# Kernel optimization log

Measured on AMD Instinct MI355X. Metric: run time of the kernel, lower is better.

The kernel has to match this reference:

```python
import jax, jax.numpy as jnp
import numpy as np


def _per_sample_ce(logits, targets):
    # -log_softmax(logits)[i, targets[i]]  -> shape [N]
    logp = jax.nn.log_softmax(logits, axis=-1)
    return -jnp.take_along_axis(logp, targets[:, None], axis=-1)[:, 0]


def setup_inputs() -> dict:
    key = jax.random.key(0)
    k1, k2, k3 = jax.random.split(key, 3)
    N, C = 65536, 1000
    y_1 = jax.random.normal(k1, (N, C), dtype=jnp.float32)
    y_2 = jax.random.normal(k2, (N, C), dtype=jnp.float32)
    targets = jax.random.randint(k3, (N,), 0, C, dtype=jnp.int64)
    num_keep = 45875  # int(0.7 * N), static for jit
    return {"y_1": y_1, "y_2": y_2, "targets": targets, "num_keep": num_keep}


def reference(y_1, y_2, targets, num_keep):
    loss_1 = _per_sample_ce(y_1, targets)          # [N]
    loss_2 = _per_sample_ce(y_2, targets)          # [N]
    # small-loss selection: indices of the num_keep smallest per-sample losses
    ind_1_update = jnp.argsort(loss_1)[:num_keep]  # selected by net 1
    ind_2_update = jnp.argsort(loss_2)[:num_keep]  # selected by net 2
    # cross-update: each net trains on the peer's selected samples
    loss_1_update = _per_sample_ce(y_1[ind_2_update], targets[ind_2_update])
    loss_2_update = _per_sample_ce(y_2[ind_1_update], targets[ind_1_update])
    # size_average=True -> means
    return (loss_1_update.mean(), loss_2_update.mean(),
            loss_1.mean(), loss_2.mean())
```

## Files before the change

kernel.cpp:

```cpp
#include <hip/hip_runtime.h>
#include <math.h>

#define MAXT 2048

__device__ __forceinline__ unsigned keyOf(float f) {
  unsigned b = __float_as_uint(f);
  return b ^ ((b & 0x80000000u) ? 0xFFFFFFFFu : 0x80000000u);
}

__device__ __forceinline__ float waveMax(float v) {
#pragma unroll
  for (int o = 32; o >= 1; o >>= 1) v = fmaxf(v, __shfl_xor(v, o));
  return v;
}
__device__ __forceinline__ float waveSum(float v) {
#pragma unroll
  for (int o = 32; o >= 1; o >>= 1) v += __shfl_xor(v, o);
  return v;
}

__device__ __forceinline__ void selectStep(const unsigned* __restrict__ h,
                                           int per, unsigned rank,
                                           unsigned* sc, unsigned* res) {
  int t = threadIdx.x;
  unsigned local[8];
  unsigned s = 0;
  for (int j = 0; j < per; ++j) { local[j] = h[t * per + j]; s += local[j]; }
  sc[t] = s;
  __syncthreads();
  for (int off = 1; off < 256; off <<= 1) {
    unsigned v = (t >= off) ? sc[t - off] : 0u;
    __syncthreads();
    sc[t] += v;
    __syncthreads();
  }
  unsigned incl = sc[t], excl = incl - s;
  if (excl < rank && rank <= incl) {
    unsigned cum = excl;
    for (int j = 0; j < per; ++j) {
      if (cum + local[j] >= rank) {
        res[0] = (unsigned)(t * per + j);
        res[1] = rank - cum;
        break;
      }
      cum += local[j];
    }
  }
  __syncthreads();
}

__global__ __launch_bounds__(256) void init_kernel(unsigned* __restrict__ hbase,
                                                   unsigned* __restrict__ tc) {
  int t = threadIdx.x;
  for (int j = t; j < 2 * (2048 + 2048 + 1024); j += 256) hbase[j] = 0u;
  if (t < 2) tc[t] = 0u;
}

__global__ __launch_bounds__(256) void ce_kernel(
    const float* __restrict__ y1, const float* __restrict__ y2,
    const int* __restrict__ tgt,
    float* __restrict__ l1, float* __restrict__ l2, int N) {
  const float L2E = 1.4426950408889634f;
  const float LN2 = 0.6931471805599453f;
  int wid = threadIdx.x >> 6, lane = threadIdx.x & 63;
  int row = blockIdx.x * 4 + wid;
  if (row >= N) return;
  int t = tgt[row];
  int vecIdx = t >> 2;
  int grp = vecIdx >> 6;
  int srcLane = vecIdx & 63;
  int comp = t & 3;
#pragma unroll
  for (int which = 0; which < 2; ++which) {
    const float* y = which ? y2 : y1;
    const float4* rp = (const float4*)(y + (size_t)row * 1000);
    float4 a = rp[lane];
    float4 b = rp[lane + 64];
    float4 c = rp[lane + 128];
    float4 d = make_float4(-INFINITY, -INFINITY, -INFINITY, -INFINITY);
    if (lane + 192 < 250) d = rp[lane + 192];
    float4 sel = (grp == 0) ? a : (grp == 1) ? b : (grp == 2) ? c : d;
    float cand = (comp == 0) ? sel.x : (comp == 1) ? sel.y
               : (comp == 2) ? sel.z : sel.w;
    float xt = __shfl(cand, srcLane);
    float m = fmaxf(fmaxf(fmaxf(a.x, a.y), fmaxf(a.z, a.w)),
                    fmaxf(fmaxf(b.x, b.y), fmaxf(b.z, b.w)));
    m = fmaxf(m, fmaxf(fmaxf(c.x, c.y), fmaxf(c.z, c.w)));
    m = fmaxf(m, fmaxf(fmaxf(d.x, d.y), fmaxf(d.z, d.w)));
    m = waveMax(m);
    float s = exp2f((a.x - m) * L2E) + exp2f((a.y - m) * L2E) +
              exp2f((a.z - m) * L2E) + exp2f((a.w - m) * L2E) +
              exp2f((b.x - m) * L2E) + exp2f((b.y - m) * L2E) +
              exp2f((b.z - m) * L2E) + exp2f((b.w - m) * L2E) +
              exp2f((c.x - m) * L2E) + exp2f((c.y - m) * L2E) +
              exp2f((c.z - m) * L2E) + exp2f((c.w - m) * L2E) +
              exp2f((d.x - m) * L2E) + exp2f((d.y - m) * L2E) +
              exp2f((d.z - m) * L2E) + exp2f((d.w - m) * L2E);
    s = waveSum(s);
    if (lane == 0) {
      float loss = log2f(s) * LN2 + m - xt;
      (which ? l2 : l1)[row] = loss;
    }
  }
}

__global__ __launch_bounds__(256) void histA_kernel(
    const float* __restrict__ l1, const float* __restrict__ l2,
    unsigned* __restrict__ hA1, unsigned* __restrict__ hA2, int N) {
  __shared__ unsigned lh[2][2048];
  int t = threadIdx.x;
  for (int j = t; j < 2048; j += 256) { lh[0][j] = 0u; lh[1][j] = 0u; }
  __syncthreads();
  for (int i = blockIdx.x * blockDim.x + t; i < N;
       i += gridDim.x * blockDim.x) {
    atomicAdd(&lh[0][keyOf(l1[i]) >> 21], 1u);
    atomicAdd(&lh[1][keyOf(l2[i]) >> 21], 1u);
  }
  __syncthreads();
  for (int j = t; j < 2048; j += 256) {
    unsigned v0 = lh[0][j], v1 = lh[1][j];
    if (v0) atomicAdd(&hA1[j], v0);
    if (v1) atomicAdd(&hA2[j], v1);
  }
}

__global__ __launch_bounds__(256) void histB_kernel(
    const float* __restrict__ l1, const float* __restrict__ l2,
    const unsigned* __restrict__ hA1, const unsigned* __restrict__ hA2,
    unsigned* __restrict__ hB1, unsigned* __restrict__ hB2,
    const int* __restrict__ numKeep, int N) {
  __shared__ unsigned sc[256];
  __shared__ unsigned resA1[2], resA2[2];
  unsigned k0 = (unsigned)(*numKeep);
  selectStep(hA1, 8, k0, sc, resA1);
  selectStep(hA2, 8, k0, sc, resA2);
  unsigned a1 = resA1[0], a2 = resA2[0];
  for (int i = blockIdx.x * blockDim.x + threadIdx.x; i < N;
       i += gridDim.x * blockDim.x) {
    unsigned k1 = keyOf(l1[i]);
    if ((k1 >> 21) == a1) atomicAdd(&hB1[(k1 >> 10) & 2047u], 1u);
    unsigned k2 = keyOf(l2[i]);
    if ((k2 >> 21) == a2) atomicAdd(&hB2[(k2 >> 10) & 2047u], 1u);
  }
}

__global__ __launch_bounds__(256) void histC_kernel(
    const float* __restrict__ l1, const float* __restrict__ l2,
    const unsigned* __restrict__ hA1, const unsigned* __restrict__ hA2,
    const unsigned* __restrict__ hB1, const unsigned* __restrict__ hB2,
    unsigned* __restrict__ hC1, unsigned* __restrict__ hC2,
    const int* __restrict__ numKeep, int N) {
  __shared__ unsigned sc[256];
  __shared__ unsigned rA1[2], rA2[2], rB1[2], rB2[2];
  unsigned k0 = (unsigned)(*numKeep);
  selectStep(hA1, 8, k0, sc, rA1);
  selectStep(hA2, 8, k0, sc, rA2);
  selectStep(hB1, 8, rA1[1], sc, rB1);
  selectStep(hB2, 8, rA2[1], sc, rB2);
  unsigned p1 = (rA1[0] << 21) | (rB1[0] << 10);
  unsigned p2 = (rA2[0] << 21) | (rB2[0] << 10);
  for (int i = blockIdx.x * blockDim.x + threadIdx.x; i < N;
       i += gridDim.x * blockDim.x) {
    unsigned k1 = keyOf(l1[i]);
    if ((k1 & 0xFFFFFC00u) == p1) atomicAdd(&hC1[k1 & 1023u], 1u);
    unsigned k2 = keyOf(l2[i]);
    if ((k2 & 0xFFFFFC00u) == p2) atomicAdd(&hC2[k2 & 1023u], 1u);
  }
}

__global__ __launch_bounds__(256) void partial_kernel(
    const float* __restrict__ l1, const float* __restrict__ l2,
    const unsigned* __restrict__ hA1, const unsigned* __restrict__ hA2,
    const unsigned* __restrict__ hB1, const unsigned* __restrict__ hB2,
    const unsigned* __restrict__ hC1, const unsigned* __restrict__ hC2,
    const int* __restrict__ numKeep, unsigned* __restrict__ needs,
    unsigned* __restrict__ tc, int* __restrict__ tIdx1, float* __restrict__ tVal1,
    int* __restrict__ tIdx2, float* __restrict__ tVal2,
    float* __restrict__ partials, int N) {
  __shared__ unsigned sc[256];
  __shared__ unsigned rA1[2], rA2[2], rB1[2], rB2[2], rC1[2], rC2[2];
  unsigned k0 = (unsigned)(*numKeep);
  selectStep(hA1, 8, k0, sc, rA1);
  selectStep(hA2, 8, k0, sc, rA2);
  selectStep(hB1, 8, rA1[1], sc, rB1);
  selectStep(hB2, 8, rA2[1], sc, rB2);
  selectStep(hC1, 4, rB1[1], sc, rC1);
  selectStep(hC2, 4, rB2[1], sc, rC2);
  unsigned K1 = (rA1[0] << 21) | (rB1[0] << 10) | rC1[0];
  unsigned K2 = (rA2[0] << 21) | (rB2[0] << 10) | rC2[0];
  if (threadIdx.x == 0) { needs[0] = rC1[1]; needs[1] = rC2[1]; }
  float s0 = 0.f, s1 = 0.f, s2 = 0.f, s3 = 0.f;
  for (int i = blockIdx.x * blockDim.x + threadIdx.x; i < N;
       i += gridDim.x * blockDim.x) {
    float f1 = l1[i], f2 = l2[i];
    unsigned k1 = keyOf(f1), k2 = keyOf(f2);
    if (k2 < K2) {
      s0 += f1;
    } else if (k2 == K2) {
      unsigned p = atomicAdd(&tc[1], 1u);
      if (p < MAXT) { tIdx2[p] = i; tVal2[p] = f1; }
    }
    if (k1 < K1) {
      s1 += f2;
    } else if (k1 == K1) {
      unsigned p = atomicAdd(&tc[0], 1u);
      if (p < MAXT) { tIdx1[p] = i; tVal1[p] = f2; }
    }
    s2 += f1;
    s3 += f2;
  }
  s0 = waveSum(s0); s1 = waveSum(s1); s2 = waveSum(s2); s3 = waveSum(s3);
  __shared__ float red[4][4];
  int wid = threadIdx.x >> 6, lane = threadIdx.x & 63;
  if (lane == 0) {
    red[wid][0] = s0; red[wid][1] = s1; red[wid][2] = s2; red[wid][3] = s3;
  }
  __syncthreads();
  if (threadIdx.x == 0) {
    for (int q = 0; q < 4; ++q)
      partials[blockIdx.x * 4 + q] =
          red[0][q] + red[1][q] + red[2][q] + red[3][q];
  }
}

__global__ __launch_bounds__(256) void final_kernel(
    const float* __restrict__ partials, const int* __restrict__ numKeep,
    const unsigned* __restrict__ needs, const unsigned* __restrict__ tc,
    const int* __restrict__ tIdx1, const float* __restrict__ tVal1,
    const int* __restrict__ tIdx2, const float* __restrict__ tVal2,
    float* __restrict__ out, int N, int nBlocks) {
  __shared__ float slots[MAXT];
  __shared__ float red[4][4];
  __shared__ float tieSum[2];
  int t = threadIdx.x;
  float s0 = 0.f, s1 = 0.f, s2 = 0.f, s3 = 0.f;
  for (int j = t; j < nBlocks; j += 256) {
    s0 += partials[j * 4 + 0];
    s1 += partials[j * 4 + 1];
    s2 += partials[j * 4 + 2];
    s3 += partials[j * 4 + 3];
  }
  s0 = waveSum(s0); s1 = waveSum(s1); s2 = waveSum(s2); s3 = waveSum(s3);
  int wid = t >> 6, lane = t & 63;
  if (lane == 0) {
    red[wid][0] = s0; red[wid][1] = s1; red[wid][2] = s2; red[wid][3] = s3;
  }
  for (int a = 0; a < 2; ++a) {
    const int* ti = a ? tIdx2 : tIdx1;
    const float* tv = a ? tVal2 : tVal1;
    int T = min((int)tc[a], MAXT);
    int need = min((int)needs[a], T);
    __syncthreads();
    for (int j = t; j < T; j += 256) {
      int idx = ti[j];
      int rk = 0;
      for (int m = 0; m < T; ++m) rk += (ti[m] < idx) ? 1 : 0;
      if (rk < need) slots[rk] = tv[j];
    }
    __syncthreads();
    if (t == 0) {
      float s = 0.f;
      for (int j = 0; j < need; ++j) s += slots[j];
      tieSum[a] = s;
    }
  }
  __syncthreads();
  if (t == 0) {
    float a0 = red[0][0] + red[1][0] + red[2][0] + red[3][0] + tieSum[1];
    float a1 = red[0][1] + red[1][1] + red[2][1] + red[3][1] + tieSum[0];
    float a2 = red[0][2] + red[1][2] + red[2][2] + red[3][2];
    float a3 = red[0][3] + red[1][3] + red[2][3] + red[3][3];
    float k = (float)(*numKeep);
    out[0] = a0 / k;
    out[1] = a1 / k;
    out[2] = a2 / (float)N;
    out[3] = a3 / (float)N;
  }
}

extern "C" void kernel_launch(void* const* d_in, const int* in_sizes, int n_in,
                              void* d_out, int out_size, void* d_ws,
                              size_t ws_size, hipStream_t stream) {
  const float* y1 = (const float*)d_in[0];
  const float* y2 = (const float*)d_in[1];
  const int* tgt = (const int*)d_in[2];
  const int* numKeep = (const int*)d_in[3];
  int N = in_sizes[2];
  float* out = (float*)d_out;

  float* l1 = (float*)d_ws;
  float* l2 = l1 + N;
  unsigned* hA1 = (unsigned*)(l2 + N);
  unsigned* hA2 = hA1 + 2048;
  unsigned* hB1 = hA2 + 2048;
  unsigned* hB2 = hB1 + 2048;
  unsigned* hC1 = hB2 + 2048;
  unsigned* hC2 = hC1 + 1024;
  unsigned* tc = hC2 + 1024;
  unsigned* needs = tc + 2;
  int* tIdx1 = (int*)(needs + 2);
  float* tVal1 = (float*)(tIdx1 + MAXT);
  int* tIdx2 = (int*)(tVal1 + MAXT);
  float* tVal2 = (float*)(tIdx2 + MAXT);
  float* partials = (float*)(tVal2 + MAXT);

  init_kernel<<<1, 256, 0, stream>>>(hA1, tc);
  ce_kernel<<<(N + 3) / 4, 256, 0, stream>>>(y1, y2, tgt, l1, l2, N);
  histA_kernel<<<256, 256, 0, stream>>>(l1, l2, hA1, hA2, N);
  histB_kernel<<<256, 256, 0, stream>>>(l1, l2, hA1, hA2, hB1, hB2, numKeep, N);
  histC_kernel<<<256, 256, 0, stream>>>(l1, l2, hA1, hA2, hB1, hB2, hC1, hC2,
                                        numKeep, N);
  partial_kernel<<<256, 256, 0, stream>>>(l1, l2, hA1, hA2, hB1, hB2, hC1, hC2,
                                          numKeep, needs, tc, tIdx1, tVal1,
                                          tIdx2, tVal2, partials, N);
  final_kernel<<<1, 256, 0, stream>>>(partials, numKeep, needs, tc, tIdx1,
                                      tVal1, tIdx2, tVal2, out, N, 256);
}
```

Baseline: 138.1 us.

## Drop histC pass, fuse final reduction into partial kernel, skip softmax max

The third radix histogram pass is removed: ties are now collected at 22-bit key-prefix granularity, and the final tie ranking sorts them by full key and then index. The final kernel is folded into partial_kernel using a last-block-done atomic counter, and the init kernel's zeroing moves into block 0 of ce_kernel. This cuts three launches and one full pass over the loss arrays. ce_kernel now issues both rows' loads up front and no longer subtracts the row max before exp, which removes a wave reduction but risks overflow for large logits.

After: 144.8 us. 1.05x slower.

```diff
diff --git a/kernel.cpp b/kernel.cpp
--- a/kernel.cpp
+++ b/kernel.cpp
@@ -8,11 +8,6 @@
   return b ^ ((b & 0x80000000u) ? 0xFFFFFFFFu : 0x80000000u);
 }
 
-__device__ __forceinline__ float waveMax(float v) {
-#pragma unroll
-  for (int o = 32; o >= 1; o >>= 1) v = fmaxf(v, __shfl_xor(v, o));
-  return v;
-}
 __device__ __forceinline__ float waveSum(float v) {
 #pragma unroll
   for (int o = 32; o >= 1; o >>= 1) v += __shfl_xor(v, o);
@@ -49,19 +44,16 @@
   __syncthreads();
 }
 
-__global__ __launch_bounds__(256) void init_kernel(unsigned* __restrict__ hbase,
-                                                   unsigned* __restrict__ tc) {
-  int t = threadIdx.x;
-  for (int j = t; j < 2 * (2048 + 2048 + 1024); j += 256) hbase[j] = 0u;
-  if (t < 2) tc[t] = 0u;
-}
-
 __global__ __launch_bounds__(256) void ce_kernel(
     const float* __restrict__ y1, const float* __restrict__ y2,
     const int* __restrict__ tgt,
-    float* __restrict__ l1, float* __restrict__ l2, int N) {
+    float* __restrict__ l1, float* __restrict__ l2,
+    unsigned* __restrict__ zeroBase, int zeroCount, int N) {
   const float L2E = 1.4426950408889634f;
   const float LN2 = 0.6931471805599453f;
+  if (blockIdx.x == 0) {
+    for (int j = threadIdx.x; j < zeroCount; j += 256) zeroBase[j] = 0u;
+  }
   int wid = threadIdx.x >> 6, lane = threadIdx.x & 63;
   int row = blockIdx.x * 4 + wid;
   if (row >= N) return;
@@ -70,37 +62,46 @@
   int grp = vecIdx >> 6;
   int srcLane = vecIdx & 63;
   int comp = t & 3;
+  const float4* rp1 = (const float4*)(y1 + (size_t)row * 1000);
+  const float4* rp2 = (const float4*)(y2 + (size_t)row * 1000);
+  float4 a1 = rp1[lane];
+  float4 b1 = rp1[lane + 64];
+  float4 c1 = rp1[lane + 128];
+  float4 a2 = rp2[lane];
+  float4 b2 = rp2[lane + 64];
+  float4 c2 = rp2[lane + 128];
+  float4 d1 = make_float4(-INFINITY, -INFINITY, -INFINITY, -INFINITY);
+  float4 d2 = d1;
+  if (lane < 58) {
+    d1 = rp1[lane + 192];
+    d2 = rp2[lane + 192];
+  }
+  float4 sel1 = (grp == 0) ? a1 : (grp == 1) ? b1 : (grp == 2) ? c1 : d1;
+  float4 sel2 = (grp == 0) ? a2 : (grp == 1) ? b2 : (grp == 2) ? c2 : d2;
+  float cand1 = (comp == 0) ? sel1.x : (comp == 1) ? sel1.y
+              : (comp == 2) ? sel1.z : sel1.w;
+  float cand2 = (comp == 0) ? sel2.x : (comp == 1) ? sel2.y
+              : (comp == 2) ? sel2.z : sel2.w;
+  float xt1 = __shfl(cand1, srcLane);
+  float xt2 = __shfl(cand2, srcLane);
+#define E_(v) exp2f((v) * L2E)
+  float s1 = (((E_(a1.x) + E_(a1.y)) + (E_(a1.z) + E_(a1.w))) +
+              ((E_(b1.x) + E_(b1.y)) + (E_(b1.z) + E_(b1.w)))) +
+             (((E_(c1.x) + E_(c1.y)) + (E_(c1.z) + E_(c1.w))) +
+              ((E_(d1.x) + E_(d1.y)) + (E_(d1.z) + E_(d1.w))));
+  float s2 = (((E_(a2.x) + E_(a2.y)) + (E_(a2.z) + E_(a2.w))) +
+              ((E_(b2.x) + E_(b2.y)) + (E_(b2.z) + E_(b2.w)))) +
+             (((E_(c2.x) + E_(c2.y)) + (E_(c2.z) + E_(c2.w))) +
+              ((E_(d2.x) + E_(d2.y)) + (E_(d2.z) + E_(d2.w))));
+#undef E_
 #pragma unroll
-  for (int which = 0; which < 2; ++which) {
-    const float* y = which ? y2 : y1;
-    const float4* rp = (const float4*)(y + (size_t)row * 1000);
-    float4 a = rp[lane];
-    float4 b = rp[lane + 64];
-    float4 c = rp[lane + 128];
-    float4 d = make_float4(-INFINITY, -INFINITY, -INFINITY, -INFINITY);
-    if (lane + 192 < 250) d = rp[lane + 192];
-    float4 sel = (grp == 0) ? a : (grp == 1) ? b : (grp == 2) ? c : d;
-    float cand = (comp == 0) ? sel.x : (comp == 1) ? sel.y
-               : (comp == 2) ? sel.z : sel.w;
-    float xt = __shfl(cand, srcLane);
-    float m = fmaxf(fmaxf(fmaxf(a.x, a.y), fmaxf(a.z, a.w)),
-                    fmaxf(fmaxf(b.x, b.y), fmaxf(b.z, b.w)));
-    m = fmaxf(m, fmaxf(fmaxf(c.x, c.y), fmaxf(c.z, c.w)));
-    m = fmaxf(m, fmaxf(fmaxf(d.x, d.y), fmaxf(d.z, d.w)));
-    m = waveMax(m);
-    float s = exp2f((a.x - m) * L2E) + exp2f((a.y - m) * L2E) +
-              exp2f((a.z - m) * L2E) + exp2f((a.w - m) * L2E) +
-              exp2f((b.x - m) * L2E) + exp2f((b.y - m) * L2E) +
-              exp2f((b.z - m) * L2E) + exp2f((b.w - m) * L2E) +
-              exp2f((c.x - m) * L2E) + exp2f((c.y - m) * L2E) +
-              exp2f((c.z - m) * L2E) + exp2f((c.w - m) * L2E) +
-              exp2f((d.x - m) * L2E) + exp2f((d.y - m) * L2E) +
-              exp2f((d.z - m) * L2E) + exp2f((d.w - m) * L2E);
-    s = waveSum(s);
-    if (lane == 0) {
-      float loss = log2f(s) * LN2 + m - xt;
-      (which ? l2 : l1)[row] = loss;
-    }
+  for (int o = 32; o >= 1; o >>= 1) {
+    s1 += __shfl_xor(s1, o);
+    s2 += __shfl_xor(s2, o);
+  }
+  if (lane == 0) {
+    l1[row] = log2f(s1) * LN2 - xt1;
+    l2[row] = log2f(s2) * LN2 - xt2;
   }
 }
 
@@ -144,12 +145,15 @@
   }
 }
 
-__global__ __launch_bounds__(256) void histC_kernel(
+__global__ __launch_bounds__(256) void partial_kernel(
     const float* __restrict__ l1, const float* __restrict__ l2,
     const unsigned* __restrict__ hA1, const unsigned* __restrict__ hA2,
     const unsigned* __restrict__ hB1, const unsigned* __restrict__ hB2,
-    unsigned* __restrict__ hC1, unsigned* __restrict__ hC2,
-    const int* __restrict__ numKeep, int N) {
+    const int* __restrict__ numKeep, unsigned* __restrict__ tc,
+    unsigned* __restrict__ done,
+    int* __restrict__ tIdx1, unsigned* __restrict__ tKey1, float* __restrict__ tVal1,
+    int* __restrict__ tIdx2, unsigned* __restrict__ tKey2, float* __restrict__ tVal2,
+    float* __restrict__ partials, float* __restrict__ out, int N) {
   __shared__ unsigned sc[256];
   __shared__ unsigned rA1[2], rA2[2], rB1[2], rB2[2];
   unsigned k0 = (unsigned)(*numKeep);
@@ -157,54 +161,25 @@
   selectStep(hA2, 8, k0, sc, rA2);
   selectStep(hB1, 8, rA1[1], sc, rB1);
   selectStep(hB2, 8, rA2[1], sc, rB2);
-  unsigned p1 = (rA1[0] << 21) | (rB1[0] << 10);
-  unsigned p2 = (rA2[0] << 21) | (rB2[0] << 10);
-  for (int i = blockIdx.x * blockDim.x + threadIdx.x; i < N;
-       i += gridDim.x * blockDim.x) {
-    unsigned k1 = keyOf(l1[i]);
-    if ((k1 & 0xFFFFFC00u) == p1) atomicAdd(&hC1[k1 & 1023u], 1u);
-    unsigned k2 = keyOf(l2[i]);
-    if ((k2 & 0xFFFFFC00u) == p2) atomicAdd(&hC2[k2 & 1023u], 1u);
-  }
-}
-
-__global__ __launch_bounds__(256) void partial_kernel(
-    const float* __restrict__ l1, const float* __restrict__ l2,
-    const unsigned* __restrict__ hA1, const unsigned* __restrict__ hA2,
-    const unsigned* __restrict__ hB1, const unsigned* __restrict__ hB2,
-    const unsigned* __restrict__ hC1, const unsigned* __restrict__ hC2,
-    const int* __restrict__ numKeep, unsigned* __restrict__ needs,
-    unsigned* __restrict__ tc, int* __restrict__ tIdx1, float* __restrict__ tVal1,
-    int* __restrict__ tIdx2, float* __restrict__ tVal2,
-    float* __restrict__ partials, int N) {
-  __shared__ unsigned sc[256];
-  __shared__ unsigned rA1[2], rA2[2], rB1[2], rB2[2], rC1[2], rC2[2];
-  unsigned k0 = (unsigned)(*numKeep);
-  selectStep(hA1, 8, k0, sc, rA1);
-  selectStep(hA2, 8, k0, sc, rA2);
-  selectStep(hB1, 8, rA1[1], sc, rB1);
-  selectStep(hB2, 8, rA2[1], sc, rB2);
-  selectStep(hC1, 4, rB1[1], sc, rC1);
-  selectStep(hC2, 4, rB2[1], sc, rC2);
-  unsigned K1 = (rA1[0] << 21) | (rB1[0] << 10) | rC1[0];
-  unsigned K2 = (rA2[0] << 21) | (rB2[0] << 10) | rC2[0];
-  if (threadIdx.x == 0) { needs[0] = rC1[1]; needs[1] = rC2[1]; }
+  unsigned P1 = (rA1[0] << 11) | rB1[0];
+  unsigned P2 = (rA2[0] << 11) | rB2[0];
   float s0 = 0.f, s1 = 0.f, s2 = 0.f, s3 = 0.f;
   for (int i = blockIdx.x * blockDim.x + threadIdx.x; i < N;
        i += gridDim.x * blockDim.x) {
     float f1 = l1[i], f2 = l2[i];
     unsigned k1 = keyOf(f1), k2 = keyOf(f2);
-    if (k2 < K2) {
+    unsigned q1 = k1 >> 10, q2 = k2 >> 10;
+    if (q2 < P2) {
       s0 += f1;
-    } else if (k2 == K2) {
+    } else if (q2 == P2) {
       unsigned p = atomicAdd(&tc[1], 1u);
-      if (p < MAXT) { tIdx2[p] = i; tVal2[p] = f1; }
-    }
-    if (k1 < K1) {
+      if (p < MAXT) { tIdx2[p] = i; tKey2[p] = k2; tVal2[p] = f1; }
+    }
+    if (q1 < P1) {
       s1 += f2;
-    } else if (k1 == K1) {
+    } else if (q1 == P1) {
       unsigned p = atomicAdd(&tc[0], 1u);
-      if (p < MAXT) { tIdx1[p] = i; tVal1[p] = f2; }
+      if (p < MAXT) { tIdx1[p] = i; tKey1[p] = k1; tVal1[p] = f2; }
     }
     s2 += f1;
     s3 += f2;
@@ -221,40 +196,44 @@
       partials[blockIdx.x * 4 + q] =
           red[0][q] + red[1][q] + red[2][q] + red[3][q];
   }
-}
-
-__global__ __launch_bounds__(256) void final_kernel(
-    const float* __restrict__ partials, const int* __restrict__ numKeep,
-    const unsigned* __restrict__ needs, const unsigned* __restrict__ tc,
-    const int* __restrict__ tIdx1, const float* __restrict__ tVal1,
-    const int* __restrict__ tIdx2, const float* __restrict__ tVal2,
-    float* __restrict__ out, int N, int nBlocks) {
+  __shared__ unsigned amLast;
+  __threadfence();
+  if (threadIdx.x == 0)
+    amLast = (atomicAdd(done, 1u) == (unsigned)(gridDim.x - 1)) ? 1u : 0u;
+  __syncthreads();
+  if (!amLast) return;
+  __threadfence();
+  int t = threadIdx.x;
+  float u0 = 0.f, u1 = 0.f, u2 = 0.f, u3 = 0.f;
+  for (int j = t; j < (int)gridDim.x; j += 256) {
+    u0 += partials[j * 4 + 0];
+    u1 += partials[j * 4 + 1];
+    u2 += partials[j * 4 + 2];
+    u3 += partials[j * 4 + 3];
+  }
+  u0 = waveSum(u0); u1 = waveSum(u1); u2 = waveSum(u2); u3 = waveSum(u3);
+  __syncthreads();
+  if (lane == 0) {
+    red[wid][0] = u0; red[wid][1] = u1; red[wid][2] = u2; red[wid][3] = u3;
+  }
   __shared__ float slots[MAXT];
-  __shared__ float red[4][4];
   __shared__ float tieSum[2];
-  int t = threadIdx.x;
-  float s0 = 0.f, s1 = 0.f, s2 = 0.f, s3 = 0.f;
-  for (int j = t; j < nBlocks; j += 256) {
-    s0 += partials[j * 4 + 0];
-    s1 += partials[j * 4 + 1];
-    s2 += partials[j * 4 + 2];
-    s3 += partials[j * 4 + 3];
-  }
-  s0 = waveSum(s0); s1 = waveSum(s1); s2 = waveSum(s2); s3 = waveSum(s3);
-  int wid = t >> 6, lane = t & 63;
-  if (lane == 0) {
-    red[wid][0] = s0; red[wid][1] = s1; red[wid][2] = s2; red[wid][3] = s3;
-  }
+  unsigned needArr[2] = {rB1[1], rB2[1]};
   for (int a = 0; a < 2; ++a) {
     const int* ti = a ? tIdx2 : tIdx1;
+    const unsigned* tk = a ? tKey2 : tKey1;
     const float* tv = a ? tVal2 : tVal1;
     int T = min((int)tc[a], MAXT);
-    int need = min((int)needs[a], T);
+    int need = min((int)needArr[a], T);
     __syncthreads();
     for (int j = t; j < T; j += 256) {
       int idx = ti[j];
+      unsigned kj = tk[j];
       int rk = 0;
-      for (int m = 0; m < T; ++m) rk += (ti[m] < idx) ? 1 : 0;
+      for (int m = 0; m < T; ++m) {
+        unsigned km = tk[m];
+        rk += (km < kj || (km == kj && ti[m] < idx)) ? 1 : 0;
+      }
       if (rk < need) slots[rk] = tv[j];
     }
     __syncthreads();
@@ -270,7 +249,7 @@
     float a1 = red[0][1] + red[1][1] + red[2][1] + red[3][1] + tieSum[0];
     float a2 = red[0][2] + red[1][2] + red[2][2] + red[3][2];
     float a3 = red[0][3] + red[1][3] + red[2][3] + red[3][3];
-    float k = (float)(*numKeep);
+    float k = (float)k0;
     out[0] = a0 / k;
     out[1] = a1 / k;
     out[2] = a2 / (float)N;
@@ -294,25 +273,21 @@
   unsigned* hA2 = hA1 + 2048;
   unsigned* hB1 = hA2 + 2048;
   unsigned* hB2 = hB1 + 2048;
-  unsigned* hC1 = hB2 + 2048;
-  unsigned* hC2 = hC1 + 1024;
-  unsigned* tc = hC2 + 1024;
-  unsigned* needs = tc + 2;
-  int* tIdx1 = (int*)(needs + 2);
-  float* tVal1 = (float*)(tIdx1 + MAXT);
+  unsigned* tc = hB2 + 2048;
+  unsigned* done = tc + 2;
+  int* tIdx1 = (int*)(done + 1);
+  unsigned* tKey1 = (unsigned*)(tIdx1 + MAXT);
+  float* tVal1 = (float*)(tKey1 + MAXT);
   int* tIdx2 = (int*)(tVal1 + MAXT);
-  float* tVal2 = (float*)(tIdx2 + MAXT);
+  unsigned* tKey2 = (unsigned*)(tIdx2 + MAXT);
+  float* tVal2 = (float*)(tKey2 + MAXT);
   float* partials = (float*)(tVal2 + MAXT);
 
-  init_kernel<<<1, 256, 0, stream>>>(hA1, tc);
-  ce_kernel<<<(N + 3) / 4, 256, 0, stream>>>(y1, y2, tgt, l1, l2, N);
+  ce_kernel<<<(N + 3) / 4, 256, 0, stream>>>(y1, y2, tgt, l1, l2, hA1,
+                                             4 * 2048 + 3, N);
   histA_kernel<<<256, 256, 0, stream>>>(l1, l2, hA1, hA2, N);
   histB_kernel<<<256, 256, 0, stream>>>(l1, l2, hA1, hA2, hB1, hB2, numKeep, N);
-  histC_kernel<<<256, 256, 0, stream>>>(l1, l2, hA1, hA2, hB1, hB2, hC1, hC2,
-                                        numKeep, N);
-  partial_kernel<<<256, 256, 0, stream>>>(l1, l2, hA1, hA2, hB1, hB2, hC1, hC2,
-                                          numKeep, needs, tc, tIdx1, tVal1,
-                                          tIdx2, tVal2, partials, N);
-  final_kernel<<<1, 256, 0, stream>>>(partials, numKeep, needs, tc, tIdx1,
-                                      tVal1, tIdx2, tVal2, out, N, 256);
-}
+  partial_kernel<<<256, 256, 0, stream>>>(l1, l2, hA1, hA2, hB1, hB2, numKeep,
+                                          tc, done, tIdx1, tKey1, tVal1, tIdx2,
+                                          tKey2, tVal2, partials, out, N);
+}
```
